# Performance work log

Hardware: AMD Instinct MI355X
Metric: run time of the kernel (lower is better)

The kernel has to match this reference:

```python
import jax, jax.numpy as jnp
from jax import lax
import numpy as np

KSIZE = 3      # match-patch size
STRIDE = 1
RATE = 2       # down/up-sampling rate
FUSE_K = 3
SCALE = 10.0   # softmax scale
DN = ('NHWC', 'HWIO', 'NHWC')


def extract_patches(x, k, s):
    """tf.image.extract_patches(..., padding='SAME'); returns [B, L, k, k, C]."""
    B, H, W, C = x.shape
    oh, ow = -(-H // s), -(-W // s)
    ph = max((oh - 1) * s + k - H, 0)
    pw = max((ow - 1) * s + k - W, 0)
    xp = jnp.pad(x, ((0, 0), (ph // 2, ph - ph // 2), (pw // 2, pw - pw // 2), (0, 0)))
    cols = [xp[:, i:i + oh * s:s, j:j + ow * s:s, :] for i in range(k) for j in range(k)]
    p = jnp.stack(cols, axis=3)                 # [B, oh, ow, k*k, C]
    return p.reshape(B, oh * ow, k, k, C)


def setup_inputs() -> dict:
    key = jax.random.key(0)
    k1, k2, k3 = jax.random.split(key, 3)
    B, H, W, C = 4, 96, 96, 64
    f = jax.random.normal(k1, (B, H, W, C), jnp.float32)
    b = jax.random.normal(k2, (B, H, W, C), jnp.float32)
    mask = jnp.zeros((B, H, W, 1), jnp.float32)          # 0 = no hole -> all patches valid
    fuse_weight = jax.random.normal(k3, (FUSE_K, FUSE_K, 1, 1), jnp.float32) * 0.3
    return {"f": f, "b": b, "mask": mask, "fuse_weight": fuse_weight}


def reference(f, b, mask, fuse_weight):
    B, H, W, C = f.shape
    kernel = 2 * RATE
    # deconv kernels from full-res background: [B, 4, 4, C, L]
    raw_w = extract_patches(b, kernel, RATE * STRIDE).transpose(0, 2, 3, 4, 1)
    fd = f[:, 1::2, 1::2, :]
    bd = b[:, 1::2, 1::2, :]
    md = mask[:, 1::2, 1::2, :]
    h, w_ = fd.shape[1], fd.shape[2]
    L = h * w_
    # matching kernels from downscaled background: [B, 3, 3, C, L]
    wk = extract_patches(bd, KSIZE, STRIDE).transpose(0, 2, 3, 4, 1)
    # mask patches -> per-patch validity mm: [B, L]
    mp = extract_patches(md, KSIZE, STRIDE)
    mm = (jnp.mean(mp, axis=(2, 3, 4)) == 0.0).astype(f.dtype)

    def per_sample(xi, wi, rwi, mmi):
        # xi: [h, w, C]; wi: [3,3,C,L]; rwi: [4,4,C,L]; mmi: [L]
        norm = jnp.maximum(jnp.sqrt(jnp.sum(wi * wi, axis=(0, 1, 2))), 1e-4)
        yi = lax.conv_general_dilated(xi[None], wi / norm, (1, 1), 'SAME',
                                      dimension_numbers=DN)[0]        # [h, w, L]
        # fuse: 3x3 conv over flattened [HW, HW] score map, twice (transposed view)
        y = yi.reshape(1, L, L, 1)
        y = lax.conv_general_dilated(y, fuse_weight, (1, 1), 'SAME', dimension_numbers=DN)
        y = y.reshape(h, w_, h, w_).transpose(1, 0, 3, 2).reshape(1, L, L, 1)
        y = lax.conv_general_dilated(y, fuse_weight, (1, 1), 'SAME', dimension_numbers=DN)
        y = y.reshape(w_, h, w_, h).transpose(1, 0, 3, 2).reshape(h, w_, L)
        # mask-gated scaled softmax over background patches
        y = y * mmi
        y = jax.nn.softmax(y * SCALE, axis=-1) * mmi
        # deconv-style combine with raw 4x4 patches, stride=rate
        out = lax.conv_transpose(y[None], rwi, (RATE, RATE), 'SAME',
                                 dimension_numbers=DN, transpose_kernel=True)[0] / 4.0
        return out                                                    # [H, W, C]

    return jax.vmap(per_sample)(fd, wk, raw_w, mm)
```

## Files before the change

kernel.cpp:

```cpp
#include <hip/hip_runtime.h>
#include <hip/hip_bf16.h>

#define KL  2304
#define KC  64
#define KHS 48
#define KHH 96
#define OFFY (KHS*(KL + 1))

typedef __attribute__((ext_vector_type(8))) short bf16x8;
typedef __attribute__((ext_vector_type(4))) short bf16x4;
typedef __attribute__((ext_vector_type(8))) _Float16 f16x8;
typedef __attribute__((ext_vector_type(4))) _Float16 f16x4;
typedef __attribute__((ext_vector_type(4))) float f32x4;

static __device__ inline unsigned short f2bf(float x) {
    __hip_bfloat16 h = __float2bfloat16(x);
    return *reinterpret_cast<unsigned short*>(&h);
}
static __device__ inline float bf2f(unsigned short u) {
    unsigned v = ((unsigned)u) << 16;
    return __uint_as_float(v);
}
static __device__ inline unsigned short f2h(float x) {
    _Float16 h = (_Float16)x;
    return *reinterpret_cast<unsigned short*>(&h);
}
static __device__ inline float h2f(unsigned short u) {
    _Float16 h = *reinterpret_cast<_Float16*>(&u);
    return (float)h;
}

__global__ __launch_bounds__(256) void k_prep2(const float* __restrict__ f,
    const float* __restrict__ bsrc, const float* __restrict__ mask,
    float* __restrict__ nbuf, float* __restrict__ mdd,
    unsigned short* __restrict__ Ahat, unsigned short* __restrict__ Bhat)
{
    int pp = blockIdx.x*4 + (threadIdx.x >> 6);
    int c = threadIdx.x & 63;
    int p = pp % KL, bi = pp / KL;
    int y = p / KHS, x = p % KHS;
    int fy = 2*y + 1;
    unsigned short* Ap = Ahat + ((size_t)bi*KL + p)*192;
    unsigned short* Bp = Bhat + ((size_t)bi*KL + p)*192;
    float bc = 0.f;
    #pragma unroll
    for (int dxi = 0; dxi < 3; dxi++) {
        int xx = x + dxi - 1;
        float av = 0.f, bv = 0.f;
        if ((unsigned)xx < KHS) {
            int fxx = 2*xx + 1;
            size_t src = (((size_t)bi*KHH + fy)*KHH + fxx)*KC + c;
            av = f[src]; bv = bsrc[src];
        }
        if (dxi == 1) bc = bv;
        Ap[dxi*64 + c] = f2h(av);
        Bp[dxi*64 + c] = f2h(bv);
    }
    float s = bc*bc;
    #pragma unroll
    for (int off = 32; off > 0; off >>= 1) s += __shfl_down(s, off);
    if (c == 0) {
        nbuf[bi*KL + p] = s;
        mdd[bi*KL + p]  = mask[((size_t)bi*KHH + fy)*KHH + (2*x + 1)];
    }
}

__global__ __launch_bounds__(256) void k_normmask(const float* __restrict__ nbuf,
    const float* __restrict__ mdd, float* __restrict__ rnrm, float* __restrict__ mm)
{
    int i = blockIdx.x*256 + threadIdx.x;
    int q = i % KL, bi = i / KL;
    int v = q / KHS, u = q % KHS;
    float sn = 0.f, sm = 0.f;
    for (int dy = -1; dy <= 1; dy++) {
        int vv = v + dy; if ((unsigned)vv >= KHS) continue;
        for (int dx = -1; dx <= 1; dx++) {
            int uu = u + dx; if ((unsigned)uu >= KHS) continue;
            sn += nbuf[bi*KL + vv*KHS + uu];
            sm += mdd[bi*KL + vv*KHS + uu];
        }
    }
    rnrm[i] = 1.0f / fmaxf(sqrtf(sn), 1e-4f);
    mm[i]   = (sm == 0.0f) ? 1.0f : 0.0f;
}

template<int KITERS, int OUTMODE, bool INFP16>
__global__ __launch_bounds__(256) void k_mfma_bt(const unsigned short* __restrict__ A,
    const unsigned short* __restrict__ B, void* __restrict__ Cv,
    int Ncols, size_t sA, size_t sB, size_t sC, int KDIM, int nsplit, size_t psize)
{
    int flat = blockIdx.x + gridDim.x*(blockIdx.y + gridDim.y*blockIdx.z);
    int nxy = gridDim.x*gridDim.y;
    int per = (nxy*gridDim.z) >> 3;
    int g = (flat & 7)*per + (flat >> 3);
    int z = g / nxy; int r = g - z*nxy;
    int by = r / gridDim.x; int bx = r - by*gridDim.x;

    int ks = z % nsplit, bi = z / nsplit;
    int kbase = ks * KITERS * 32;
    int n0 = bx*128, m0 = by*128;
    const unsigned short* Ab = A + (size_t)bi*sA;
    const unsigned short* Bb = B + (size_t)bi*sB;
    __shared__ unsigned short As[128*32];
    __shared__ unsigned short Bs[128*32];
    int t = threadIdx.x;
    int lane = t & 63, w = t >> 6;
    int l15 = lane & 15, quad = lane >> 4;
    int swf = (l15 >> 2) & 3;
    int wm = (w >> 1)*64, wn = (w & 1)*64;
    int srow = lane >> 2;
    int ch = lane & 3;
    f32x4 acc[4][4];
    #pragma unroll
    for (int i = 0; i < 4; i++)
        #pragma unroll
        for (int j = 0; j < 4; j++) acc[i][j] = (f32x4){0.f,0.f,0.f,0.f};

    for (int kk = 0; kk < KITERS; kk++) {
        int k0 = kbase + kk*32;
        #pragma unroll
        for (int i = 0; i < 2; i++) {
            int rbase = w*32 + i*16;
            int r2 = rbase + srow;
            int cs = (ch ^ ((r2 >> 2) & 3))*8;
            const unsigned short* ga = &Ab[(size_t)(m0 + r2)*KDIM + k0 + cs];
            __builtin_amdgcn_global_load_lds(
                (const __attribute__((address_space(1))) void*)ga,
                (__attribute__((address_space(3))) void*)&As[rbase*32], 16, 0, 0);
            const unsigned short* gb = &Bb[(size_t)(n0 + r2)*KDIM + k0 + cs];
            __builtin_amdgcn_global_load_lds(
                (const __attribute__((address_space(1))) void*)gb,
                (__attribute__((address_space(3))) void*)&Bs[rbase*32], 16, 0, 0);
        }
        __syncthreads();
        if (INFP16) {
            f16x8 af[4], bfr[4];
            #pragma unroll
            for (int mi = 0; mi < 4; mi++)
                af[mi] = *(const f16x8*)&As[(wm + mi*16 + l15)*32 + ((quad ^ swf)*8)];
            #pragma unroll
            for (int ni = 0; ni < 4; ni++)
                bfr[ni] = *(const f16x8*)&Bs[(wn + ni*16 + l15)*32 + ((quad ^ swf)*8)];
            #pragma unroll
            for (int mi = 0; mi < 4; mi++)
                #pragma unroll
                for (int ni = 0; ni < 4; ni++)
                    acc[mi][ni] = __builtin_amdgcn_mfma_f32_16x16x32_f16(
                        af[mi], bfr[ni], acc[mi][ni], 0, 0, 0);
        } else {
            bf16x8 af[4], bfr[4];
            #pragma unroll
            for (int mi = 0; mi < 4; mi++)
                af[mi] = *(const bf16x8*)&As[(wm + mi*16 + l15)*32 + ((quad ^ swf)*8)];
            #pragma unroll
            for (int ni = 0; ni < 4; ni++)
                bfr[ni] = *(const bf16x8*)&Bs[(wn + ni*16 + l15)*32 + ((quad ^ swf)*8)];
            #pragma unroll
            for (int mi = 0; mi < 4; mi++)
                #pragma unroll
                for (int ni = 0; ni < 4; ni++)
                    acc[mi][ni] = __builtin_amdgcn_mfma_f32_16x16x32_bf16(
                        af[mi], bfr[ni], acc[mi][ni], 0, 0, 0);
        }
        __syncthreads();
    }
    if (OUTMODE == 1 || OUTMODE == 2) {
        unsigned short* Cb = (unsigned short*)Cv + (size_t)ks*psize + (size_t)bi*sC;
        #pragma unroll
        for (int mi = 0; mi < 4; mi++)
            #pragma unroll
            for (int ni = 0; ni < 4; ni++) {
                int col = n0 + wn + ni*16 + l15;
                #pragma unroll
                for (int r2 = 0; r2 < 4; r2++) {
                    int row = m0 + wm + mi*16 + quad*4 + r2;
                    Cb[(size_t)row*Ncols + col] = (OUTMODE == 1)
                        ? f2bf(acc[mi][ni][r2]) : f2h(acc[mi][ni][r2]);
                }
            }
    } else {
        float* Cb = (float*)Cv + (size_t)ks*psize + (size_t)bi*sC;
        #pragma unroll
        for (int mi = 0; mi < 4; mi++)
            #pragma unroll
            for (int ni = 0; ni < 4; ni++) {
                int col = n0 + wn + ni*16 + l15;
                #pragma unroll
                for (int r2 = 0; r2 < 4; r2++) {
                    int row = m0 + wm + mi*16 + quad*4 + r2;
                    Cb[(size_t)row*Ncols + col] = acc[mi][ni][r2];
                }
            }
    }
}

#define KP_NT 24
#define STGA4(tt, j) do {                                                      \
    __builtin_amdgcn_global_load_lds(                                          \
        (const __attribute__((address_space(1))) void*)(gA + (size_t)(j)*128*2304 + (size_t)(tt)*32), \
        (__attribute__((address_space(3))) void*)&Atile[(tt)&3][((j)*128 + (w<<4))*32], 16, 0, 0); \
} while (0)

#define BLD(tt, BV) do {                                                       \
    _Pragma("unroll")                                                          \
    for (int ni = 0; ni < 4; ni++) {                                           \
        const unsigned short* _a = gBn[ni] + (size_t)(tt)*32;                  \
        asm volatile("global_load_dwordx4 %0, %1, off"                         \
                     : "=v"(BV[ni]) : "v"(_a));                                \
    }                                                                          \
} while (0)

#define MFMA_B(a, b, c) __builtin_amdgcn_mfma_f32_16x16x32_bf16(a, b, c, 0, 0, 0)

#define KT_BODY(kt, BVU) do {                                                  \
    const unsigned short* At = &Atile[(kt) & 3][0];                            \
    __builtin_amdgcn_s_barrier();                                              \
    _Pragma("unroll")                                                          \
    for (int i = 0; i < 4; i++)                                                \
        af1[i] = *(const bf16x8*)&At[aOff + 2048 + i*512];                     \
    if ((kt) + 3 < KP_NT) { STGA4((kt)+3, 0); STGA4((kt)+3, 1); }              \
    if ((kt) <= KP_NT-4)      asm volatile("s_waitcnt vmcnt(8)" ::: "memory"); \
    else if ((kt) == KP_NT-3) asm volatile("s_waitcnt vmcnt(6)" ::: "memory"); \
    else if ((kt) == KP_NT-2) asm volatile("s_waitcnt vmcnt(4)" ::: "memory"); \
    else                      asm volatile("s_waitcnt vmcnt(0)" ::: "memory"); \
    __builtin_amdgcn_sched_barrier(0);                                         \
    __builtin_amdgcn_s_setprio(1);                                             \
    _Pragma("unroll")                                                          \
    for (int mi = 0; mi < 4; mi++)                                             \
        _Pragma("unroll")                                                      \
        for (int ni = 0; ni < 4; ni++)                                         \
            acc[mi][ni] = MFMA_B(af0[mi], BVU[ni], acc[mi][ni]);               \
    __builtin_amdgcn_s_setprio(0);                                             \
    if ((kt) < KP_NT-1) {                                                      \
        const unsigned short* An = &Atile[((kt)+1) & 3][0];                    \
        _Pragma("unroll")                                                      \
        for (int i = 0; i < 4; i++)                                            \
            af0[i] = *(const bf16x8*)&An[aOff + i*512];                        \
    }                                                                          \
    __builtin_amdgcn_s_setprio(1);                                             \
    _Pragma("unroll")                                                          \
    for (int mi = 0; mi < 4; mi++)                                             \
        _Pragma("unroll")                                                      \
        for (int ni = 0; ni < 4; ni++)                                         \
            acc[4+mi][ni] = MFMA_B(af1[mi], BVU[ni], acc[4+mi][ni]);           \
    __builtin_amdgcn_s_setprio(0);                                             \
    if ((kt) + 2 < KP_NT) { BLD((kt)+2, BVU); }                                \
} while (0)

__global__ __launch_bounds__(512, 2) void k_p8(
    const unsigned short* __restrict__ A,
    const unsigned short* __restrict__ B,
    unsigned short* __restrict__ C,
    size_t psize)
{
    __shared__ unsigned short Atile[4][8192];

    int flat = blockIdx.x + gridDim.x*(blockIdx.y + gridDim.y*blockIdx.z);
    int nwg = gridDim.x*gridDim.y*gridDim.z;
    int qq = nwg >> 3, rr8 = nwg & 7;
    int xcd = flat & 7, sub = flat >> 3;
    int g = (xcd < rr8 ? xcd*(qq+1) : rr8*(qq+1) + (xcd - rr8)*qq) + sub;
    int nxy = gridDim.x*gridDim.y;
    int z = g / nxy; int rg = g - z*nxy;
    int by = rg / gridDim.x; int bx = rg - by*gridDim.x;

    int ks = z % 3, bi = z / 3;
    int kbase = ks * 768;
    int m0 = by * 256, n0 = bx * 256;
    const unsigned short* Ab = A + (size_t)bi * (2304ull*2304);
    const unsigned short* Bb = B + (size_t)bi * (1024ull*2304);

    int t = threadIdx.x;
    int w = t >> 6, lane = t & 63;
    int wr = w >> 2, wc = w & 3;
    int l15 = lane & 15, quad = lane >> 4;

    int scol = ((t & 3) ^ ((t >> 3) & 3))*8;
    const unsigned short* gA = Ab + (size_t)(m0 + (t >> 2))*2304 + kbase + scol;

    const unsigned short* gBn[4];
    #pragma unroll
    for (int ni = 0; ni < 4; ni++)
        gBn[ni] = Bb + (size_t)(n0 + wc*64 + ni*16 + l15)*2304 + kbase + quad*8;

    int csw = (quad ^ ((l15 >> 1) & 3))*8;
    int aOff = (wr*128 + l15)*32 + csw;

    f32x4 acc[8][4];
    #pragma unroll
    for (int mi = 0; mi < 8; mi++)
        #pragma unroll
        for (int ni = 0; ni < 4; ni++) acc[mi][ni] = (f32x4){0.f,0.f,0.f,0.f};

    bf16x8 af0[4], af1[4], bvA[4], bvB[4];

    STGA4(0, 0); STGA4(0, 1);
    STGA4(1, 0); STGA4(1, 1);
    STGA4(2, 0); STGA4(2, 1);
    BLD(0, bvA);
    BLD(1, bvB);
    asm volatile("s_waitcnt vmcnt(4)" ::: "memory");
    __builtin_amdgcn_sched_barrier(0);
    __builtin_amdgcn_s_barrier();
    #pragma unroll
    for (int i = 0; i < 4; i++)
        af0[i] = *(const bf16x8*)&Atile[0][aOff + i*512];

    #pragma unroll 1
    for (int ktp = 0; ktp < KP_NT/2; ktp++) {
        int kt0 = ktp*2;
        KT_BODY(kt0,     bvA);
        KT_BODY(kt0 + 1, bvB);
    }

    unsigned short* Cb = C + (size_t)ks*psize + (size_t)bi*(2304ull*1024);
    #pragma unroll
    for (int mi = 0; mi < 8; mi++)
        #pragma unroll
        for (int ni = 0; ni < 4; ni++) {
            int col = n0 + wc*64 + ni*16 + l15;
            int rowb = m0 + wr*128 + mi*16 + quad*4;
            #pragma unroll
            for (int r = 0; r < 4; r++)
                Cb[(size_t)(rowb + r)*1024 + col] = f2bf(acc[mi][ni][r]);
        }
}

__global__ __launch_bounds__(256) void k_fuse_a2(const unsigned short* __restrict__ T,
    const float* __restrict__ rnrm, const float* __restrict__ fw,
    unsigned short* __restrict__ Y1)
{
    __shared__ float Sl[10][280];
    int flat = blockIdx.x + 9*(blockIdx.y + 288*blockIdx.z);
    int nwg = 2592*gridDim.z;
    int cpx = nwg >> 3;
    int g = (flat & 7)*cpx + (flat >> 3);
    int bi = g / 2592; int rem = g - bi*2592;
    int by = rem / 9;  int qt = rem - by*9;

    int p0 = by*8, q0 = qt*256;
    const unsigned short* Tb = T + (size_t)bi*KL*KL;
    const float* rn = rnrm + bi*KL;
    int t = threadIdx.x;
    bool edge = (qt == 0) | (qt == 8);
    if (!edge) {
        for (int idx = t; idx < 10*34; idx += 256) {
            int r = idx / 34, j = idx - r*34;
            int pp = p0 - 1 + r;
            int qq0 = q0 - 8 + j*8;
            float s[8];
            #pragma unroll
            for (int k = 0; k < 8; k++) s[k] = 0.f;
            if ((unsigned)pp < KL) {
                size_t base = (size_t)pp*KL + qq0;
                bool bm = (pp >= KHS), bp = (pp < KL - KHS);
                size_t offm = bm ? (size_t)OFFY : 0;
                size_t offp = bp ? (size_t)OFFY : 0;
                float fm = bm ? 1.f : 0.f, fp2 = bp ? 1.f : 0.f;
                f16x8 v0 = *(const f16x8*)&Tb[base];
                f16x8 vm = *(const f16x8*)&Tb[base - offm];
                f16x8 vp = *(const f16x8*)&Tb[base + offp];
                #pragma unroll
                for (int k = 0; k < 8; k++)
                    s[k] = ((float)v0[k] + fm*(float)vm[k] + fp2*(float)vp[k]) * rn[qq0 + k];
            }
            #pragma unroll
            for (int k = 0; k < 8; k++) Sl[r][j*8 + k] = s[k];
        }
    } else {
        for (int idx = t; idx < 10*272; idx += 256) {
            int r = idx / 272, c = idx - r*272;
            int pp = p0 - 1 + r, qq = q0 - 8 + c;
            float s = 0.f;
            if ((unsigned)pp < KL && (unsigned)qq < KL) {
                size_t base = (size_t)pp*KL + qq;
                float acc = h2f(Tb[base]);
                if (pp >= KHS && qq >= KHS)         acc += h2f(Tb[base - OFFY]);
                if (pp < KL - KHS && qq < KL - KHS) acc += h2f(Tb[base + OFFY]);
                s = acc * rn[qq];
            }
            Sl[r][c] = s;
        }
    }
    __syncthreads();
    float w[9];
    #pragma unroll
    for (int i = 0; i < 9; i++) w[i] = fw[i];
    int q = q0 + t;
    float h0[10], h1[10], h2[10];
    #pragma unroll
    for (int r = 0; r < 10; r++) {
        float s0 = Sl[r][t+7], s1 = Sl[r][t+8], s2 = Sl[r][t+9];
        h0[r] = w[0]*s0 + w[1]*s1 + w[2]*s2;
        h1[r] = w[3]*s0 + w[4]*s1 + w[5]*s2;
        h2[r] = w[6]*s0 + w[7]*s1 + w[8]*s2;
    }
    #pragma unroll
    for (int rr = 0; rr < 8; rr++) {
        Y1[((size_t)bi*KL + p0 + rr)*KL + q] = f2h(h0[rr] + h1[rr+1] + h2[rr+2]);
    }
}

__global__ __launch_bounds__(256) void k_fuse_b(const unsigned short* __restrict__ Y1,
    const float* __restrict__ fw, const float* __restrict__ mm,
    unsigned short* __restrict__ Ybf)
{
    __shared__ float rowb[6][KL];
    int blk = blockIdx.x;
    int tp0 = (blk % 576)*4;
    int bi  = blk / 576;
    int t = threadIdx.x;
    const unsigned short* Yb = Y1 + (size_t)bi*KL*KL;
    for (int idx = t; idx < 6*(KL/8); idx += 256) {
        int a = idx / (KL/8), i = idx - a*(KL/8);
        int t2 = tp0 - 1 + a;
        if ((unsigned)t2 < KL) {
            int pr = (t2 % KHS)*KHS + t2/KHS;
            f16x8 v = *(const f16x8*)&Yb[(size_t)pr*KL + i*8];
            #pragma unroll
            for (int j = 0; j < 8; j++) rowb[a][i*8 + j] = (float)v[j];
        } else {
            #pragma unroll
            for (int j = 0; j < 8; j++) rowb[a][i*8 + j] = 0.f;
        }
    }
    float w9[9];
    #pragma unroll
    for (int i = 0; i < 9; i++) w9[i] = fw[i];
    __syncthreads();
    int w = t >> 6, lane = t & 63;
    int tp = tp0 + w;
    int x = tp / KHS, y = tp - x*KHS;
    int p = y*KHS + x;
    const float* mmb = mm + bi*KL;
    float vals[36];
    float lmax = -1e30f;
    #pragma unroll
    for (int i = 0; i < 36; i++) {
        int q = lane + i*64;
        int qm = (q >= KHS)      ? q - KHS : 2255 + q;
        int qp = (q <= KL-1-KHS) ? q + KHS : q - 2255;
        float fm = (q != 0)    ? 1.f : 0.f;
        float fp = (q != KL-1) ? 1.f : 0.f;
        float am = w9[0]*rowb[w][qm] + w9[3]*rowb[w+1][qm] + w9[6]*rowb[w+2][qm];
        float a0 = w9[1]*rowb[w][q]  + w9[4]*rowb[w+1][q]  + w9[7]*rowb[w+2][q];
        float ap = w9[2]*rowb[w][qp] + w9[5]*rowb[w+1][qp] + w9[8]*rowb[w+2][qp];
        float val = (fm*am + a0 + fp*ap) * mmb[q] * 10.0f;
        vals[i] = val;
        lmax = fmaxf(lmax, val);
    }
    #pragma unroll
    for (int off = 32; off > 0; off >>= 1) lmax = fmaxf(lmax, __shfl_down(lmax, off));
    lmax = __shfl(lmax, 0);
    float lsum = 0.f;
    #pragma unroll
    for (int i = 0; i < 36; i++) {
        float e = __expf(vals[i] - lmax);
        vals[i] = e;
        lsum += e;
    }
    #pragma unroll
    for (int off = 32; off > 0; off >>= 1) lsum += __shfl_down(lsum, off);
    lsum = __shfl(lsum, 0);
    float inv = 1.0f / lsum;
    unsigned short* orow = Ybf + ((size_t)bi*KL + p)*KL;
    #pragma unroll
    for (int i = 0; i < 36; i++) {
        int q = lane + i*64;
        orow[q] = f2bf(vals[i]*inv*mmb[q]);
    }
}

__global__ __launch_bounds__(256) void k_buildRt(const float* __restrict__ bsrc,
    unsigned short* __restrict__ Rt)
{
    int idx = blockIdx.x*256 + threadIdx.x;
    int k8 = idx % 288;
    int rest = idx / 288;
    int n  = rest % 1024;
    int bi = rest / 1024;
    int jj = n >> 6, c = n & 63;
    int ky = jj >> 2, kx = jj & 3;
    int k0 = k8*8;
    bf16x8 vv;
    #pragma unroll
    for (int j = 0; j < 8; j++) {
        int q = k0 + j;
        int v = q / KHS, u = q % KHS;
        int ry = 2*v + ky - 1, rx = 2*u + kx - 1;
        float val = 0.f;
        if ((unsigned)ry < KHH && (unsigned)rx < KHH)
            val = bsrc[(((size_t)bi*KHH + ry)*KHH + rx)*KC + c];
        vv[j] = (short)f2bf(val);
    }
    *(bf16x8*)&Rt[((size_t)bi*1024 + n)*KL + k0] = vv;
}

__global__ __launch_bounds__(256) void k_overlap(const unsigned short* __restrict__ P,
    float* __restrict__ out, size_t psize)
{
    size_t gid = (size_t)blockIdx.x*256 + threadIdx.x;
    int c4 = (int)(gid & 15)*4;
    size_t r = gid >> 4;
    int ix = (int)(r % KHH); r /= KHH;
    int iy = (int)(r % KHH);
    int bi = (int)(r / KHH);
    f32x4 acc = (f32x4){0.f,0.f,0.f,0.f};
    #pragma unroll
    for (int sy = 0; sy < 2; sy++) {
        int ky = (iy & 1) ? (sy*2) : (sy*2 + 1);
        int yp = (iy + 1 - ky) >> 1;
        if ((unsigned)yp >= KHS) continue;
        #pragma unroll
        for (int sx = 0; sx < 2; sx++) {
            int kx = (ix & 1) ? (sx*2) : (sx*2 + 1);
            int xp = (ix + 1 - kx) >> 1;
            if ((unsigned)xp >= KHS) continue;
            size_t idx = (((size_t)bi*KL + yp*KHS + xp)*16 + (ky*4 + kx))*64 + c4;
            #pragma unroll
            for (int s = 0; s < 3; s++) {
                bf16x4 v = *(const bf16x4*)&P[idx + s*psize];
                #pragma unroll
                for (int j = 0; j < 4; j++)
                    acc[j] += bf2f((unsigned short)v[j]);
            }
        }
    }
    f32x4 o = acc * 0.25f;
    *(f32x4*)&out[(((size_t)bi*KHH + iy)*KHH + ix)*KC + c4] = o;
}

extern "C" void kernel_launch(void* const* d_in, const int* in_sizes, int n_in,
                              void* d_out, int out_size, void* d_ws, size_t ws_size,
                              hipStream_t stream)
{
    const float* f    = (const float*)d_in[0];
    const float* b    = (const float*)d_in[1];
    const float* mask = (const float*)d_in[2];
    const float* fw   = (const float*)d_in[3];
    float* out = (float*)d_out;

    auto need = [](int nbc) -> size_t {
        return (size_t)nbc * (2ull*KL*KC + 4ull*KL + 2ull*(size_t)KL*KL) * 4ull;
    };
    int nbc = 4;
    if (need(nbc) > ws_size) nbc = 2;
    if (need(nbc) > ws_size) nbc = 1;

    for (int bi0 = 0; bi0 < 4; bi0 += nbc) {
        int nb = (4 - bi0 < nbc) ? (4 - bi0) : nbc;
        const float* fc = f    + (size_t)bi0*KHH*KHH*KC;
        const float* bc = b    + (size_t)bi0*KHH*KHH*KC;
        const float* mc = mask + (size_t)bi0*KHH*KHH;
        float* outc = out + (size_t)bi0*KHH*KHH*KC;

        float* w    = (float*)d_ws;
        float* nbuf = w;  w += (size_t)nbc*KL;
        float* mdd  = w;  w += (size_t)nbc*KL;
        float* rnrm = w;  w += (size_t)nbc*KL;
        float* mmb  = w;  w += (size_t)nbc*KL;
        float* bufA = w;  w += (size_t)nbc*KL*KL;
        float* bufB = w;
        unsigned short* Ahat = (unsigned short*)bufB;
        unsigned short* Bhat = Ahat + (size_t)nbc*KL*192;
        unsigned short* Tbuf = (unsigned short*)bufA;
        unsigned short* Y1   = (unsigned short*)bufB;
        unsigned short* Ybf = (unsigned short*)bufA;
        unsigned short* Rtb = Ybf + (size_t)nbc*KL*KL;
        unsigned short* Pbuf = (unsigned short*)bufB;
        size_t psize = (size_t)nbc*KL*1024;

        k_prep2     <<<nb*KL/4, 256, 0, stream>>>(fc, bc, mc, nbuf, mdd, Ahat, Bhat);
        k_normmask  <<<(nb*KL)/256, 256, 0, stream>>>(nbuf, mdd, rnrm, mmb);
        k_mfma_bt<6,2,true><<<dim3(18, 18, nb), 256, 0, stream>>>(
            Ahat, Bhat, Tbuf, KL, (size_t)KL*192, (size_t)KL*192, (size_t)KL*KL,
            192, 1, 0);
        k_fuse_a2   <<<dim3(9, 288, nb), 256, 0, stream>>>(Tbuf, rnrm, fw, Y1);
        k_fuse_b    <<<nb*576, 256, 0, stream>>>(Y1, fw, mmb, Ybf);
        k_buildRt   <<<(nb*1024*288)/256, 256, 0, stream>>>(bc, Rtb);
        k_p8<<<dim3(4, 9, nb*3), 512, 0, stream>>>(Ybf, Rtb, Pbuf, psize);
        k_overlap   <<<nb*KL/4*16/16, 256, 0, stream>>>(Pbuf, outc, psize);
    }
}
```

Baseline: 288.2 us.

## Stage B tiles through LDS with double-buffered A/B and simpler k-loop

The batched GEMM kernel k_p8 now loads B tiles into shared memory with global_load_lds, where before each lane read them from global memory straight into registers. A and B each use a two-deep LDS ring in place of the four-deep A-only ring. The unrolled two-stage KT_BODY pipeline becomes a plain loop: read all fragments, barrier, issue the prefetch, then run the MFMAs. The launch bound asks for 4 blocks per CU; this buys B data reuse across waves and lower register pressure at the cost of shallower prefetch and more barriers.

```diff
diff --git a/kernel.cpp b/kernel.cpp
--- a/kernel.cpp
+++ b/kernel.cpp
@@ -195,65 +195,28 @@
 }
 
 #define KP_NT 24
-#define STGA4(tt, j) do {                                                      \
+#define STGA2(tt, j) do {                                                      \
     __builtin_amdgcn_global_load_lds(                                          \
         (const __attribute__((address_space(1))) void*)(gA + (size_t)(j)*128*2304 + (size_t)(tt)*32), \
-        (__attribute__((address_space(3))) void*)&Atile[(tt)&3][((j)*128 + (w<<4))*32], 16, 0, 0); \
+        (__attribute__((address_space(3))) void*)&Atile[(tt)&1][((j)*128 + (w<<4))*32], 16, 0, 0); \
 } while (0)
-
-#define BLD(tt, BV) do {                                                       \
-    _Pragma("unroll")                                                          \
-    for (int ni = 0; ni < 4; ni++) {                                           \
-        const unsigned short* _a = gBn[ni] + (size_t)(tt)*32;                  \
-        asm volatile("global_load_dwordx4 %0, %1, off"                         \
-                     : "=v"(BV[ni]) : "v"(_a));                                \
-    }                                                                          \
+#define STGB2(tt, j) do {                                                      \
+    __builtin_amdgcn_global_load_lds(                                          \
+        (const __attribute__((address_space(1))) void*)(gB + (size_t)(j)*128*2304 + (size_t)(tt)*32), \
+        (__attribute__((address_space(3))) void*)&Btile[(tt)&1][((j)*128 + (w<<4))*32], 16, 0, 0); \
 } while (0)
+#define STG2(tt) do { STGA2(tt,0); STGA2(tt,1); STGB2(tt,0); STGB2(tt,1); } while (0)
 
 #define MFMA_B(a, b, c) __builtin_amdgcn_mfma_f32_16x16x32_bf16(a, b, c, 0, 0, 0)
 
-#define KT_BODY(kt, BVU) do {                                                  \
-    const unsigned short* At = &Atile[(kt) & 3][0];                            \
-    __builtin_amdgcn_s_barrier();                                              \
-    _Pragma("unroll")                                                          \
-    for (int i = 0; i < 4; i++)                                                \
-        af1[i] = *(const bf16x8*)&At[aOff + 2048 + i*512];                     \
-    if ((kt) + 3 < KP_NT) { STGA4((kt)+3, 0); STGA4((kt)+3, 1); }              \
-    if ((kt) <= KP_NT-4)      asm volatile("s_waitcnt vmcnt(8)" ::: "memory"); \
-    else if ((kt) == KP_NT-3) asm volatile("s_waitcnt vmcnt(6)" ::: "memory"); \
-    else if ((kt) == KP_NT-2) asm volatile("s_waitcnt vmcnt(4)" ::: "memory"); \
-    else                      asm volatile("s_waitcnt vmcnt(0)" ::: "memory"); \
-    __builtin_amdgcn_sched_barrier(0);                                         \
-    __builtin_amdgcn_s_setprio(1);                                             \
-    _Pragma("unroll")                                                          \
-    for (int mi = 0; mi < 4; mi++)                                             \
-        _Pragma("unroll")                                                      \
-        for (int ni = 0; ni < 4; ni++)                                         \
-            acc[mi][ni] = MFMA_B(af0[mi], BVU[ni], acc[mi][ni]);               \
-    __builtin_amdgcn_s_setprio(0);                                             \
-    if ((kt) < KP_NT-1) {                                                      \
-        const unsigned short* An = &Atile[((kt)+1) & 3][0];                    \
-        _Pragma("unroll")                                                      \
-        for (int i = 0; i < 4; i++)                                            \
-            af0[i] = *(const bf16x8*)&An[aOff + i*512];                        \
-    }                                                                          \
-    __builtin_amdgcn_s_setprio(1);                                             \
-    _Pragma("unroll")                                                          \
-    for (int mi = 0; mi < 4; mi++)                                             \
-        _Pragma("unroll")                                                      \
-        for (int ni = 0; ni < 4; ni++)                                         \
-            acc[4+mi][ni] = MFMA_B(af1[mi], BVU[ni], acc[4+mi][ni]);           \
-    __builtin_amdgcn_s_setprio(0);                                             \
-    if ((kt) + 2 < KP_NT) { BLD((kt)+2, BVU); }                                \
-} while (0)
-
-__global__ __launch_bounds__(512, 2) void k_p8(
+__global__ __launch_bounds__(512, 4) void k_p8(
     const unsigned short* __restrict__ A,
     const unsigned short* __restrict__ B,
     unsigned short* __restrict__ C,
     size_t psize)
 {
-    __shared__ unsigned short Atile[4][8192];
+    __shared__ unsigned short Atile[2][8192];
+    __shared__ unsigned short Btile[2][8192];
 
     int flat = blockIdx.x + gridDim.x*(blockIdx.y + gridDim.y*blockIdx.z);
     int nwg = gridDim.x*gridDim.y*gridDim.z;
@@ -277,14 +240,11 @@
 
     int scol = ((t & 3) ^ ((t >> 3) & 3))*8;
     const unsigned short* gA = Ab + (size_t)(m0 + (t >> 2))*2304 + kbase + scol;
-
-    const unsigned short* gBn[4];
-    #pragma unroll
-    for (int ni = 0; ni < 4; ni++)
-        gBn[ni] = Bb + (size_t)(n0 + wc*64 + ni*16 + l15)*2304 + kbase + quad*8;
+    const unsigned short* gB = Bb + (size_t)(n0 + (t >> 2))*2304 + kbase + scol;
 
     int csw = (quad ^ ((l15 >> 1) & 3))*8;
     int aOff = (wr*128 + l15)*32 + csw;
+    int bOff = (wc*64  + l15)*32 + csw;
 
     f32x4 acc[8][4];
     #pragma unroll
@@ -292,25 +252,40 @@
         #pragma unroll
         for (int ni = 0; ni < 4; ni++) acc[mi][ni] = (f32x4){0.f,0.f,0.f,0.f};
 
-    bf16x8 af0[4], af1[4], bvA[4], bvB[4];
-
-    STGA4(0, 0); STGA4(0, 1);
-    STGA4(1, 0); STGA4(1, 1);
-    STGA4(2, 0); STGA4(2, 1);
-    BLD(0, bvA);
-    BLD(1, bvB);
+    STG2(0);
+    STG2(1);
     asm volatile("s_waitcnt vmcnt(4)" ::: "memory");
     __builtin_amdgcn_sched_barrier(0);
     __builtin_amdgcn_s_barrier();
-    #pragma unroll
-    for (int i = 0; i < 4; i++)
-        af0[i] = *(const bf16x8*)&Atile[0][aOff + i*512];
 
     #pragma unroll 1
-    for (int ktp = 0; ktp < KP_NT/2; ktp++) {
-        int kt0 = ktp*2;
-        KT_BODY(kt0,     bvA);
-        KT_BODY(kt0 + 1, bvB);
+    for (int kt = 0; kt < KP_NT; kt++) {
+        const unsigned short* At = &Atile[kt & 1][0];
+        const unsigned short* Bt = &Btile[kt & 1][0];
+        bf16x8 af[8], bv[4];
+        #pragma unroll
+        for (int i = 0; i < 8; i++)
+            af[i] = *(const bf16x8*)&At[aOff + i*512];
+        #pragma unroll
+        for (int ni = 0; ni < 4; ni++)
+            bv[ni] = *(const bf16x8*)&Bt[bOff + ni*512];
+        asm volatile("s_waitcnt lgkmcnt(0)" ::: "memory");
+        __builtin_amdgcn_sched_barrier(0);
+        __builtin_amdgcn_s_barrier();
+        if (kt + 2 < KP_NT) STG2(kt + 2);
+        __builtin_amdgcn_s_setprio(1);
+        #pragma unroll
+        for (int mi = 0; mi < 8; mi++)
+            #pragma unroll
+            for (int ni = 0; ni < 4; ni++)
+                acc[mi][ni] = MFMA_B(af[mi], bv[ni], acc[mi][ni]);
+        __builtin_amdgcn_s_setprio(0);
+        if (kt + 1 < KP_NT) {
+            if (kt + 2 < KP_NT) asm volatile("s_waitcnt vmcnt(4)" ::: "memory");
+            else                asm volatile("s_waitcnt vmcnt(0)" ::: "memory");
+            __builtin_amdgcn_sched_barrier(0);
+            __builtin_amdgcn_s_barrier();
+        }
     }
 
     unsigned short* Cb = C + (size_t)ks*psize + (size_t)bi*(2304ull*1024);
```

New measurement: 647.5 us. 125% more time.
